# Kernel tuning notes

Measured on AMD Instinct MI355X. Metric: run time of the kernel, lower is better.

Reference implementation:

```python
import jax, jax.numpy as jnp
import numpy as np
import math

D_MODEL = 1024
D_STATE = 64
D_CONV = 4
HEADDIM = 64
EXPAND = 2
NGROUPS = 1
D_INNER = EXPAND * D_MODEL            # 2048
NHEADS = D_INNER // HEADDIM           # 32
CONV_DIM = D_INNER + 2 * NGROUPS * D_STATE   # 2176
D_IN_PROJ = 2 * D_INNER + 2 * NGROUPS * D_STATE + NHEADS  # 4256
BATCH, SEQLEN = 2, 1024
RMS_EPS = 1.1920929e-07  # torch.finfo(float32).eps (nn.RMSNorm default)


def setup_inputs() -> dict:
    key = jax.random.key(0)
    ks = jax.random.split(key, 8)
    x = jax.random.normal(ks[0], (BATCH, SEQLEN, D_MODEL), dtype=jnp.float32)
    W_in = jax.random.normal(ks[1], (D_IN_PROJ, D_MODEL), dtype=jnp.float32) / math.sqrt(D_MODEL)
    conv_w = jax.random.normal(ks[2], (CONV_DIM, D_CONV), dtype=jnp.float32) / math.sqrt(D_CONV)
    conv_b = jnp.zeros((CONV_DIM,), dtype=jnp.float32)
    # dt_bias init as in the module: inverse-softplus of log-uniform dt
    dt_min, dt_max = 1e-3, 1e-1
    dt = jnp.exp(jax.random.uniform(ks[3], (NHEADS,)) * (math.log(dt_max) - math.log(dt_min)) + math.log(dt_min))
    dt = jnp.clip(dt, 1e-4, None)
    dt_bias = dt + jnp.log(-jnp.expm1(-dt))
    A_log = jnp.log(jax.random.uniform(ks[4], (NHEADS,), minval=1.0, maxval=16.0))
    D_param = jnp.ones((NHEADS,), dtype=jnp.float32)
    norm_w = jnp.ones((D_INNER,), dtype=jnp.float32)
    W_out = jax.random.normal(ks[5], (D_MODEL, D_INNER), dtype=jnp.float32) / math.sqrt(D_INNER)
    return {"x": x, "W_in": W_in, "conv_w": conv_w, "conv_b": conv_b,
            "dt_bias": dt_bias, "A_log": A_log, "D_param": D_param,
            "norm_w": norm_w, "W_out": W_out}


def reference(x, W_in, conv_w, conv_b, dt_bias, A_log, D_param, norm_w, W_out):
    B, L, _ = x.shape
    # input projection: z | xBC | dt_raw
    zxbcdt = x @ W_in.T                                   # (B, L, D_IN_PROJ)
    z = zxbcdt[..., :D_INNER]
    xBC = zxbcdt[..., D_INNER:D_INNER + CONV_DIM]
    dt_raw = zxbcdt[..., D_INNER + CONV_DIM:]
    dt = jax.nn.softplus(dt_raw + dt_bias)                # (B, L, H)

    # depthwise causal conv (left-pad d_conv-1, keep first L outputs)
    xpad = jnp.pad(xBC, ((0, 0), (D_CONV - 1, 0), (0, 0)))
    conv_out = conv_b
    for k in range(D_CONV):  # tiny fixed kernel width
        conv_out = conv_out + xpad[:, k:k + L, :] * conv_w[:, k]
    xBC_conv = jax.nn.silu(conv_out)                      # (B, L, CONV_DIM)

    x_ssm = xBC_conv[..., :D_INNER]
    B_ssm = xBC_conv[..., D_INNER:D_INNER + NGROUPS * D_STATE]
    C_ssm = xBC_conv[..., D_INNER + NGROUPS * D_STATE:]

    x_heads = x_ssm.reshape(B, L, NHEADS, HEADDIM)        # (B, L, H, P)
    hpg = NHEADS // NGROUPS
    B_h = jnp.repeat(B_ssm.reshape(B, L, NGROUPS, D_STATE), hpg, axis=2)  # (B, L, H, N)
    C_h = jnp.repeat(C_ssm.reshape(B, L, NGROUPS, D_STATE), hpg, axis=2)

    A = -jnp.exp(A_log)                                   # (H,)
    dA = jnp.exp(dt * A)                                  # (B, L, H)

    # selective SSM scan: h_t = dA_t * h_{t-1} + dt_t * x_t (outer) B_t ; y_t = h_t . C_t
    def step(h, inp):
        dA_t, dt_t, x_t, B_t, C_t = inp   # (B,H), (B,H), (B,H,P), (B,H,N), (B,H,N)
        h = h * dA_t[:, :, None, None] + (dt_t[:, :, None] * x_t)[..., None] * B_t[:, :, None, :]
        y = jnp.einsum('bhpn,bhn->bhp', h, C_t)
        return h, y

    h0 = jnp.zeros((B, NHEADS, HEADDIM, D_STATE), x.dtype)
    xs = (dA.swapaxes(0, 1), dt.swapaxes(0, 1), x_heads.swapaxes(0, 1),
          B_h.swapaxes(0, 1), C_h.swapaxes(0, 1))
    _, ys = jax.lax.scan(step, h0, xs)                    # ys: (L, B, H, P)
    y_heads = ys.swapaxes(0, 1) + D_param[None, None, :, None] * x_heads

    y = y_heads.reshape(B, L, D_INNER)
    # RMSNorm then SiLU(z) gate
    var = jnp.mean(y * y, axis=-1, keepdims=True)
    y = y * jax.lax.rsqrt(var + RMS_EPS) * norm_w
    y = y * jax.nn.silu(z)
    return y @ W_out.T                                    # (B, L, D_MODEL)
```

## Files before the change

### kernel.cpp

```cpp
#include <hip/hip_runtime.h>
#include <hip/hip_bf16.h>
#include <math.h>

#define D_MODEL   1024
#define D_INNER   2048
#define NHEADS    32
#define HEADDIM   64
#define D_STATE   64
#define CONV_DIM  2176
#define D_IN_PROJ 4256
#define ZXLD      4352
#define BATCH     2
#define SEQLEN    1024
#define BL        (BATCH * SEQLEN)
#define RMS_EPS   1.1920929e-07f

#define QCHUNK 64
#define NC     (SEQLEN / QCHUNK)

typedef __attribute__((ext_vector_type(8))) short short8;
typedef __attribute__((ext_vector_type(4))) float f32x4;
typedef __attribute__((ext_vector_type(8))) unsigned short ushort8v;
typedef __attribute__((ext_vector_type(4))) unsigned short ushort4v;

__device__ __forceinline__ unsigned short f2bf(float f) {
    unsigned u = __builtin_bit_cast(unsigned, f);
    unsigned r = u + 0x7FFFu + ((u >> 16) & 1u);
    return (unsigned short)(r >> 16);
}
__device__ __forceinline__ float bf2f(unsigned short u) {
    unsigned v = ((unsigned)u) << 16;
    return __builtin_bit_cast(float, v);
}
__device__ __forceinline__ void gload_lds16(const void* g, void* l) {
    __builtin_amdgcn_global_load_lds(
        (const __attribute__((address_space(1))) void*)g,
        (__attribute__((address_space(3))) void*)l, 16, 0, 0);
}

#define MFMA_BF16 __builtin_amdgcn_mfma_f32_16x16x32_bf16

template<int BM, int BN, int WR, int WC, bool OBF16>
__global__ __launch_bounds__(256) void gemm_bf16_nt(
    const unsigned short* __restrict__ A, const unsigned short* __restrict__ B,
    void* __restrict__ Cv, int K, int ldc)
{
    constexpr int RM = BM / WR;
    constexpr int RN = BN / WC;
    constexpr int MF = RM / 16;
    constexpr int NF = RN / 16;
    constexpr int GA = BM / 32;
    constexpr int GB = BN / 32;

    __shared__ unsigned short As[BM][64];
    __shared__ unsigned short Bs[BN][64];

    const int tid  = threadIdx.x;
    const int lane = tid & 63;
    const int w    = tid >> 6;
    const int wm   = w / WC;
    const int wn   = w % WC;
    const int m0   = blockIdx.y * BM;
    const int n0   = blockIdx.x * BN;

    const int srow  = lane >> 3;
    const int sslot = (lane & 7) ^ srow;

    const int fr  = lane & 15;
    const int h   = lane >> 4;
    const int fr7 = fr & 7;

    f32x4 acc[MF][NF];
#pragma unroll
    for (int mi = 0; mi < MF; ++mi)
#pragma unroll
        for (int ni = 0; ni < NF; ++ni) acc[mi][ni] = (f32x4){0.f, 0.f, 0.f, 0.f};

    for (int k0 = 0; k0 < K; k0 += 64) {
        __syncthreads();
#pragma unroll
        for (int q = 0; q < GA; ++q) {
            const int g8 = (w * GA + q) * 8;
            const unsigned short* gp =
                A + (size_t)(m0 + g8 + srow) * K + k0 + sslot * 8;
            gload_lds16(gp, &As[g8][0]);
        }
#pragma unroll
        for (int q = 0; q < GB; ++q) {
            const int g8 = (w * GB + q) * 8;
            const unsigned short* gp =
                B + (size_t)(n0 + g8 + srow) * K + k0 + sslot * 8;
            gload_lds16(gp, &Bs[g8][0]);
        }
        __syncthreads();

#pragma unroll
        for (int ks = 0; ks < 2; ++ks) {
            const int slot = (ks * 4 + h) ^ fr7;
            short8 av[MF], bv[NF];
#pragma unroll
            for (int mi = 0; mi < MF; ++mi)
                av[mi] = *(const short8*)&As[wm * RM + mi * 16 + fr][slot * 8];
#pragma unroll
            for (int ni = 0; ni < NF; ++ni)
                bv[ni] = *(const short8*)&Bs[wn * RN + ni * 16 + fr][slot * 8];
#pragma unroll
            for (int mi = 0; mi < MF; ++mi)
#pragma unroll
                for (int ni = 0; ni < NF; ++ni)
                    acc[mi][ni] = MFMA_BF16(av[mi], bv[ni], acc[mi][ni], 0, 0, 0);
        }
    }

    const int crow = (lane >> 4) * 4;
    const int ccol = lane & 15;
#pragma unroll
    for (int mi = 0; mi < MF; ++mi)
#pragma unroll
        for (int ni = 0; ni < NF; ++ni) {
            const int row0 = m0 + wm * RM + mi * 16 + crow;
            const int col  = n0 + wn * RN + ni * 16 + ccol;
#pragma unroll
            for (int r = 0; r < 4; ++r) {
                if constexpr (OBF16) {
                    ((unsigned short*)Cv)[(size_t)(row0 + r) * ldc + col] =
                        f2bf(acc[mi][ni][r]);
                } else {
                    ((float*)Cv)[(size_t)(row0 + r) * ldc + col] = acc[mi][ni][r];
                }
            }
        }
}

__global__ __launch_bounds__(256) void cast_bf16_kernel(
    const float* __restrict__ src, unsigned short* __restrict__ dst, int n4)
{
    const int i = (blockIdx.x * 256 + threadIdx.x);
    if (i >= n4) return;
    float4 v = *(const float4*)(src + (size_t)i * 4);
    ushort4 o;
    o.x = f2bf(v.x); o.y = f2bf(v.y); o.z = f2bf(v.z); o.w = f2bf(v.w);
    *(ushort4*)(dst + (size_t)i * 4) = o;
}

__global__ __launch_bounds__(256) void cast_win_pad_kernel(
    const float* __restrict__ src, unsigned short* __restrict__ dst)
{
    const int i = (blockIdx.x * 256 + threadIdx.x);
    if (i >= ZXLD * D_MODEL / 4) return;
    const int e0 = i * 4;
    const int row = e0 >> 10;
    ushort4 o = {0, 0, 0, 0};
    if (row < D_IN_PROJ) {
        float4 v = *(const float4*)(src + (size_t)e0);
        o.x = f2bf(v.x); o.y = f2bf(v.y); o.z = f2bf(v.z); o.w = f2bf(v.w);
    }
    *(ushort4*)(dst + (size_t)e0) = o;
}

__global__ __launch_bounds__(256) void dt_softplus_kernel(
    const unsigned short* __restrict__ zxb, const float* __restrict__ dt_bias,
    float* __restrict__ dtt)
{
    const int idx = blockIdx.x * 256 + threadIdx.x;
    const int m = idx >> 5;
    const int hd = idx & 31;
    const int b = m >> 10;
    const int l = m & (SEQLEN - 1);
    const float v = bf2f(zxb[(size_t)m * ZXLD + (D_INNER + CONV_DIM) + hd]) + dt_bias[hd];
    const float sp = (v > 20.f) ? v : log1pf(__expf(v));
    dtt[((size_t)b * NHEADS + hd) * SEQLEN + l] = sp;
}

__global__ __launch_bounds__(256) void conv_pre_kernel(
    const unsigned short* __restrict__ zxb,
    const float* __restrict__ conv_w, const float* __restrict__ conv_b,
    unsigned short* __restrict__ xTb, unsigned short* __restrict__ Bcc,
    unsigned short* __restrict__ BTc, unsigned short* __restrict__ Ccc)
{
    const int c = blockIdx.x;
    const int g = blockIdx.y;
    const int b = blockIdx.z;
    const int tid = threadIdx.x;

    __shared__ unsigned short L[64][138];

    const int l0 = c * QCHUNK;
    const int grow0 = b * SEQLEN + l0;
    const int r = tid >> 2;
    const int q = (tid & 3) * 16;

    for (int hh = 0; hh < 2; ++hh) {
        const int chbase = g * 128 + hh * 64;
        float in[4][16];
#pragma unroll
        for (int k = 0; k < 4; ++k) {
            const int ll = l0 + r - 3 + k;
            if (ll >= 0) {
                const unsigned short* src =
                    zxb + (size_t)(grow0 + r - 3 + k) * ZXLD + (D_INNER + chbase + q);
                ushort8v v0 = *(const ushort8v*)(src);
                ushort8v v1 = *(const ushort8v*)(src + 8);
#pragma unroll
                for (int j = 0; j < 8; ++j) { in[k][j] = bf2f(v0[j]); in[k][8 + j] = bf2f(v1[j]); }
            } else {
#pragma unroll
                for (int j = 0; j < 16; ++j) in[k][j] = 0.f;
            }
        }
        unsigned short o[16];
#pragma unroll
        for (int j = 0; j < 16; ++j) {
            const int ch = chbase + q + j;
            const float4 wv = *(const float4*)(conv_w + ch * 4);
            float a = conv_b[ch];
            a = fmaf(in[0][j], wv.x, a);
            a = fmaf(in[1][j], wv.y, a);
            a = fmaf(in[2][j], wv.z, a);
            a = fmaf(in[3][j], wv.w, a);
            o[j] = f2bf(a / (1.f + __expf(-a)));
        }

        const bool isB = (g == 16) && (hh == 0);
        const bool isC = (g == 16) && (hh == 1);
        const size_t ctile = ((size_t)b * NC + c) * 4096;

        if (isB || isC) {
            unsigned short* dst = (isB ? Bcc : Ccc) + ctile + (size_t)r * 64 + q;
            ushort8v w0, w1;
#pragma unroll
            for (int j = 0; j < 8; ++j) { w0[j] = o[j]; w1[j] = o[8 + j]; }
            *(ushort8v*)dst = w0;
            *(ushort8v*)(dst + 8) = w1;
        }
        if (!isC) {
#pragma unroll
            for (int j = 0; j < 8; ++j) { L[r][q + j] = o[j]; L[r][q + 8 + j] = o[8 + j]; }
            __syncthreads();
            const int cc = tid >> 2;
            const int tseg = (tid & 3) * 16;
            unsigned short tv[16];
#pragma unroll
            for (int j = 0; j < 16; ++j) tv[j] = L[tseg + j][cc];
            unsigned short* dstT;
            if (isB) dstT = BTc + ctile + (size_t)cc * 64 + tseg;
            else {
                const int hgt = g * 2 + hh;
                dstT = xTb + (((size_t)b * NHEADS + hgt) * NC + c) * 4096 + (size_t)cc * 64 + tseg;
            }
            ushort8v w0, w1;
#pragma unroll
            for (int j = 0; j < 8; ++j) { w0[j] = tv[j]; w1[j] = tv[8 + j]; }
            *(ushort8v*)dstT = w0;
            *(ushort8v*)(dstT + 8) = w1;
        }
        __syncthreads();
    }
}

__global__ __launch_bounds__(256) void chunk_state_kernel(
    const unsigned short* __restrict__ xTb, const unsigned short* __restrict__ BTc,
    const float* __restrict__ dtt, const float* __restrict__ A_log,
    unsigned short* __restrict__ Sintra, float* __restrict__ cumA)
{
    const int bid = blockIdx.x;
    const int c = bid & (NC - 1);
    const int h = (bid >> 4) & (NHEADS - 1);
    const int b = bid >> 9;
    const int tid = threadIdx.x;
    const int lane = tid & 63;
    const int w = tid >> 6;

    __shared__ unsigned short sXT[64][72];
    __shared__ unsigned short sBT[64][72];
    __shared__ float sw[64];

    if (tid < QCHUNK) {
        const float A = -__expf(A_log[h]);
        const float dtv = dtt[((size_t)b * NHEADS + h) * SEQLEN + c * QCHUNK + tid];
        float cum = dtv * A;
#pragma unroll
        for (int off = 1; off < 64; off <<= 1) {
            const float o = __shfl_up(cum, off, 64);
            if (tid >= off) cum += o;
        }
        const float cum_end = __shfl(cum, 63, 64);
        sw[tid] = __expf(cum_end - cum) * dtv;
        cumA[(size_t)bid * QCHUNK + tid] = cum;
    }
    __syncthreads();

    {
        const int r = tid >> 2, q = (tid & 3) * 16;
        const unsigned short* xs =
            xTb + (((size_t)b * NHEADS + h) * NC + c) * 4096 + (size_t)r * 64 + q;
        ushort8v v0 = *(const ushort8v*)(xs);
        ushort8v v1 = *(const ushort8v*)(xs + 8);
        ushort8v s0, s1;
#pragma unroll
        for (int j = 0; j < 8; ++j) {
            s0[j] = f2bf(bf2f(v0[j]) * sw[q + j]);
            s1[j] = f2bf(bf2f(v1[j]) * sw[q + 8 + j]);
        }
        *(ushort8v*)&sXT[r][q] = s0;
        *(ushort8v*)&sXT[r][q + 8] = s1;

        const unsigned short* bs =
            BTc + ((size_t)b * NC + c) * 4096 + (size_t)r * 64 + q;
        *(ushort8v*)&sBT[r][q]     = *(const ushort8v*)(bs);
        *(ushort8v*)&sBT[r][q + 8] = *(const ushort8v*)(bs + 8);
    }
    __syncthreads();

    const int fr = lane & 15;
    const int ko = (lane >> 4) * 8;
    short8 a0 = *(const short8*)&sBT[w * 16 + fr][ko];
    short8 a1 = *(const short8*)&sBT[w * 16 + fr][ko + 32];

    unsigned short* sout = Sintra + (size_t)bid * (D_STATE * HEADDIM);
    const int nrow = w * 16 + (lane >> 4) * 4;
#pragma unroll
    for (int j = 0; j < 4; ++j) {
        short8 b0 = *(const short8*)&sXT[j * 16 + fr][ko];
        short8 b1 = *(const short8*)&sXT[j * 16 + fr][ko + 32];
        f32x4 a = (f32x4){0.f, 0.f, 0.f, 0.f};
        a = MFMA_BF16(a0, b0, a, 0, 0, 0);
        a = MFMA_BF16(a1, b1, a, 0, 0, 0);
        const int p = j * 16 + fr;
#pragma unroll
        for (int r = 0; r < 4; ++r)
            sout[(size_t)(nrow + r) * HEADDIM + p] = f2bf(a[r]);
    }
}

__global__ __launch_bounds__(256) void state_pass_kernel(
    unsigned short* __restrict__ S, const float* __restrict__ cumA)
{
    const int gid = blockIdx.x * 256 + threadIdx.x;
    const int bh = gid >> 10;
    const int e0 = (gid & 1023) * 4;

    float run[4] = {0.f, 0.f, 0.f, 0.f};
    unsigned short* base = S + (size_t)bh * NC * (D_STATE * HEADDIM) + e0;

    ushort4v pre = *(const ushort4v*)base;
    float gpre = __expf(cumA[((size_t)bh * NC) * QCHUNK + (QCHUNK - 1)]);

    for (int c = 0; c < NC; ++c) {
        const ushort4v cur = pre;
        const float g = gpre;
        if (c + 1 < NC) {
            pre = *(const ushort4v*)(base + (size_t)(c + 1) * (D_STATE * HEADDIM));
            gpre = __expf(cumA[((size_t)bh * NC + c + 1) * QCHUNK + (QCHUNK - 1)]);
        }
        ushort4v o;
#pragma unroll
        for (int j = 0; j < 4; ++j) o[j] = f2bf(run[j]);
        *(ushort4v*)(base + (size_t)c * (D_STATE * HEADDIM)) = o;
#pragma unroll
        for (int j = 0; j < 4; ++j) run[j] = fmaf(g, run[j], bf2f(cur[j]));
    }
}

__global__ __launch_bounds__(256) void chunk_output_kernel(
    const unsigned short* __restrict__ xTb, const unsigned short* __restrict__ Bcc,
    const unsigned short* __restrict__ Ccc, const float* __restrict__ dtt,
    const unsigned short* __restrict__ SP, const float* __restrict__ cumA,
    const float* __restrict__ D_param, unsigned short* __restrict__ y)
{
    const int bid = blockIdx.x;
    const int c = bid & (NC - 1);
    const int h = (bid >> 4) & (NHEADS - 1);
    const int b = bid >> 9;
    const int tid = threadIdx.x;
    const int lane = tid & 63;
    const int w = tid >> 6;

    __shared__ unsigned short sC[64][72];
    __shared__ unsigned short sB[64][72];
    __shared__ unsigned short sXT[64][72];
    __shared__ unsigned short sSPT[64][72];
    __shared__ unsigned short sM[64][72];
    __shared__ float scum[64], sdt[64];

    const size_t ctile = ((size_t)b * NC + c) * 4096;
    {
        const int r = tid >> 2, q = (tid & 3) * 16;
        const unsigned short* cs = Ccc + ctile + (size_t)r * 64 + q;
        *(ushort8v*)&sC[r][q]     = *(const ushort8v*)(cs);
        *(ushort8v*)&sC[r][q + 8] = *(const ushort8v*)(cs + 8);
        const unsigned short* bs = Bcc + ctile + (size_t)r * 64 + q;
        *(ushort8v*)&sB[r][q]     = *(const ushort8v*)(bs);
        *(ushort8v*)&sB[r][q + 8] = *(const ushort8v*)(bs + 8);
        const unsigned short* xs =
            xTb + (((size_t)b * NHEADS + h) * NC + c) * 4096 + (size_t)r * 64 + q;
        *(ushort8v*)&sXT[r][q]     = *(const ushort8v*)(xs);
        *(ushort8v*)&sXT[r][q + 8] = *(const ushort8v*)(xs + 8);
        const unsigned short* ss = SP + (size_t)bid * (D_STATE * HEADDIM) + (size_t)r * 64 + q;
        ushort8v v0 = *(const ushort8v*)(ss);
        ushort8v v1 = *(const ushort8v*)(ss + 8);
#pragma unroll
        for (int j = 0; j < 8; ++j) { sSPT[q + j][r] = v0[j]; sSPT[q + 8 + j][r] = v1[j]; }
    }
    if (tid < QCHUNK) {
        scum[tid] = cumA[(size_t)bid * QCHUNK + tid];
        sdt[tid] = dtt[((size_t)b * NHEADS + h) * SEQLEN + c * QCHUNK + tid];
    }
    __syncthreads();

    const int fr = lane & 15;
    const int ko = (lane >> 4) * 8;
    const int trow = w * 16 + (lane >> 4) * 4;

    short8 aC0 = *(const short8*)&sC[w * 16 + fr][ko];
    short8 aC1 = *(const short8*)&sC[w * 16 + fr][ko + 32];

    f32x4 g[4];
#pragma unroll
    for (int j = 0; j < 4; ++j) {
        short8 b0 = *(const short8*)&sB[j * 16 + fr][ko];
        short8 b1 = *(const short8*)&sB[j * 16 + fr][ko + 32];
        f32x4 a = (f32x4){0.f, 0.f, 0.f, 0.f};
        a = MFMA_BF16(aC0, b0, a, 0, 0, 0);
        a = MFMA_BF16(aC1, b1, a, 0, 0, 0);
        g[j] = a;
    }

    float ct[4];
#pragma unroll
    for (int r = 0; r < 4; ++r) ct[r] = scum[trow + r];
#pragma unroll
    for (int j = 0; j < 4; ++j) {
        const int s = j * 16 + fr;
        const float cs = scum[s], ds = sdt[s];
#pragma unroll
        for (int r = 0; r < 4; ++r) {
            const int t = trow + r;
            const float m = (s <= t) ? g[j][r] * __expf(ct[r] - cs) * ds : 0.f;
            sM[t][s] = f2bf(m);
        }
    }
    __syncthreads();

    short8 aM0 = *(const short8*)&sM[w * 16 + fr][ko];
    short8 aM1 = *(const short8*)&sM[w * 16 + fr][ko + 32];
    f32x4 y1[4], y2[4];
#pragma unroll
    for (int j = 0; j < 4; ++j) {
        short8 bx0 = *(const short8*)&sXT[j * 16 + fr][ko];
        short8 bx1 = *(const short8*)&sXT[j * 16 + fr][ko + 32];
        f32x4 a = (f32x4){0.f, 0.f, 0.f, 0.f};
        a = MFMA_BF16(aM0, bx0, a, 0, 0, 0);
        a = MFMA_BF16(aM1, bx1, a, 0, 0, 0);
        y1[j] = a;
        short8 bs0 = *(const short8*)&sSPT[j * 16 + fr][ko];
        short8 bs1 = *(const short8*)&sSPT[j * 16 + fr][ko + 32];
        f32x4 a2 = (f32x4){0.f, 0.f, 0.f, 0.f};
        a2 = MFMA_BF16(aC0, bs0, a2, 0, 0, 0);
        a2 = MFMA_BF16(aC1, bs1, a2, 0, 0, 0);
        y2[j] = a2;
    }

    const float Dp = D_param[h];
    float et[4];
#pragma unroll
    for (int r = 0; r < 4; ++r) et[r] = __expf(ct[r]);
    unsigned short* ybase = y + (((size_t)b * SEQLEN + c * QCHUNK) * D_INNER) + h * HEADDIM;
#pragma unroll
    for (int j = 0; j < 4; ++j) {
        const int p = j * 16 + fr;
#pragma unroll
        for (int r = 0; r < 4; ++r) {
            const int t = trow + r;
            const float xv = bf2f(sXT[p][t]);
            ybase[(size_t)t * D_INNER + p] = f2bf(y1[j][r] + et[r] * y2[j][r] + Dp * xv);
        }
    }
}

__global__ __launch_bounds__(256) void rms_gate_kernel(
    const unsigned short* __restrict__ y, const unsigned short* __restrict__ zxb,
    const float* __restrict__ norm_w, unsigned short* __restrict__ out)
{
    const int m = blockIdx.x;
    const int tid = threadIdx.x;
    const unsigned short* yr = y + (size_t)m * D_INNER;
    const unsigned short* zr = zxb + (size_t)m * ZXLD;

    ushort8v yv8 = *(const ushort8v*)(yr + tid * 8);
    float yv[8];
#pragma unroll
    for (int j = 0; j < 8; ++j) yv[j] = bf2f(yv8[j]);
    float ss = 0.f;
#pragma unroll
    for (int j = 0; j < 8; ++j) ss += yv[j] * yv[j];
#pragma unroll
    for (int off = 32; off > 0; off >>= 1) ss += __shfl_xor(ss, off, 64);
    __shared__ float sred[4];
    if ((tid & 63) == 0) sred[tid >> 6] = ss;
    __syncthreads();
    const float tot = sred[0] + sred[1] + sred[2] + sred[3];
    const float inv = rsqrtf(tot * (1.f / D_INNER) + RMS_EPS);

    ushort8v zv8 = *(const ushort8v*)(zr + tid * 8);
    const float* nw = norm_w + tid * 8;
    ushort8v o;
#pragma unroll
    for (int j = 0; j < 8; ++j) {
        const float zz = bf2f(zv8[j]);
        const float sig = 1.f / (1.f + __expf(-zz));
        o[j] = f2bf(yv[j] * inv * nw[j] * (zz * sig));
    }
    *(ushort8v*)(out + (size_t)m * D_INNER + tid * 8) = o;
}

extern "C" void kernel_launch(void* const* d_in, const int* in_sizes, int n_in,
                              void* d_out, int out_size, void* d_ws, size_t ws_size,
                              hipStream_t stream)
{
    const float* x       = (const float*)d_in[0];
    const float* W_in    = (const float*)d_in[1];
    const float* conv_w  = (const float*)d_in[2];
    const float* conv_b  = (const float*)d_in[3];
    const float* dt_bias = (const float*)d_in[4];
    const float* A_log   = (const float*)d_in[5];
    const float* D_param = (const float*)d_in[6];
    const float* norm_w  = (const float*)d_in[7];
    const float* W_out   = (const float*)d_in[8];
    float* out = (float*)d_out;

    char* p = (char*)d_ws;
    unsigned short* zxb   = (unsigned short*)p;  p += (size_t)BL * ZXLD * 2;
    float*          dtt   = (float*)p;           p += (size_t)BATCH * NHEADS * SEQLEN * 4;
    float*          cumA  = (float*)p;           p += (size_t)BATCH * NHEADS * SEQLEN * 4;
    unsigned short* Sb    = (unsigned short*)p;  p += (size_t)BATCH * NHEADS * NC * 4096 * 2;
    unsigned short* xTb   = (unsigned short*)p;  p += (size_t)BATCH * NHEADS * NC * 4096 * 2;
    unsigned short* Bcc   = (unsigned short*)p;  p += (size_t)BATCH * NC * 4096 * 2;
    unsigned short* BTc   = (unsigned short*)p;  p += (size_t)BATCH * NC * 4096 * 2;
    unsigned short* Ccc   = (unsigned short*)p;  p += (size_t)BATCH * NC * 4096 * 2;
    unsigned short* ybb   = (unsigned short*)p;  p += (size_t)BL * D_INNER * 2;
    unsigned short* xb    = (unsigned short*)p;  p += (size_t)BL * D_MODEL * 2;
    unsigned short* winb  = (unsigned short*)p;  p += (size_t)ZXLD * D_MODEL * 2;
    unsigned short* woutb = (unsigned short*)p;  p += (size_t)D_MODEL * D_INNER * 2;
    unsigned short* ygb   = (unsigned short*)p;

    cast_bf16_kernel<<<(BL * D_MODEL / 4 + 255) / 256, 256, 0, stream>>>(
        x, xb, BL * D_MODEL / 4);
    cast_win_pad_kernel<<<(ZXLD * D_MODEL / 4 + 255) / 256, 256, 0, stream>>>(W_in, winb);
    cast_bf16_kernel<<<(D_MODEL * D_INNER / 4 + 255) / 256, 256, 0, stream>>>(
        W_out, woutb, D_MODEL * D_INNER / 4);

    gemm_bf16_nt<128, 128, 2, 2, true><<<dim3(ZXLD / 128, BL / 128), 256, 0, stream>>>(
        xb, winb, zxb, D_MODEL, ZXLD);

    dt_softplus_kernel<<<(BL * NHEADS) / 256, 256, 0, stream>>>(zxb, dt_bias, dtt);
    conv_pre_kernel<<<dim3(NC, 17, BATCH), 256, 0, stream>>>(
        zxb, conv_w, conv_b, xTb, Bcc, BTc, Ccc);
    chunk_state_kernel<<<BATCH * NHEADS * NC, 256, 0, stream>>>(
        xTb, BTc, dtt, A_log, Sb, cumA);
    state_pass_kernel<<<256, 256, 0, stream>>>(Sb, cumA);
    chunk_output_kernel<<<BATCH * NHEADS * NC, 256, 0, stream>>>(
        xTb, Bcc, Ccc, dtt, Sb, cumA, D_param, ybb);
    rms_gate_kernel<<<BL, 256, 0, stream>>>(ybb, zxb, norm_w, ygb);

    gemm_bf16_nt<64, 64, 2, 2, false><<<dim3(D_MODEL / 64, BL / 64), 256, 0, stream>>>(
        ygb, woutb, out, D_INNER, D_MODEL);
}
```

Baseline: 113.9 us.

## Double-buffer GEMM LDS tiles, fuse casts and fold softplus into conv kernel

The GEMM now keeps two LDS buffers and issues the next K-tile's global-to-LDS loads before computing the current tile, so loads overlap MFMA work with a single barrier per step. The three fp32-to-bf16 cast kernels become one launch, and the dt softplus kernel becomes an extra grid slice of the conv kernel. Together these cut kernel launches and hide load latency. The cost is doubled LDS per block, which can lower occupancy for the 128x128 tile configuration.

```diff
diff --git a/kernel.cpp b/kernel.cpp
--- a/kernel.cpp
+++ b/kernel.cpp
@@ -52,8 +52,8 @@
     constexpr int GA = BM / 32;
     constexpr int GB = BN / 32;
 
-    __shared__ unsigned short As[BM][64];
-    __shared__ unsigned short Bs[BN][64];
+    __shared__ unsigned short As[2][BM][64];
+    __shared__ unsigned short Bs[2][BN][64];
 
     const int tid  = threadIdx.x;
     const int lane = tid & 63;
@@ -67,7 +67,7 @@
     const int sslot = (lane & 7) ^ srow;
 
     const int fr  = lane & 15;
-    const int h   = lane >> 4;
+    const int hq  = lane >> 4;
     const int fr7 = fr & 7;
 
     f32x4 acc[MF][NF];
@@ -76,39 +76,48 @@
 #pragma unroll
         for (int ni = 0; ni < NF; ++ni) acc[mi][ni] = (f32x4){0.f, 0.f, 0.f, 0.f};
 
-    for (int k0 = 0; k0 < K; k0 += 64) {
-        __syncthreads();
+    auto stage = [&](int buf, int k0) {
 #pragma unroll
         for (int q = 0; q < GA; ++q) {
             const int g8 = (w * GA + q) * 8;
-            const unsigned short* gp =
-                A + (size_t)(m0 + g8 + srow) * K + k0 + sslot * 8;
-            gload_lds16(gp, &As[g8][0]);
+            gload_lds16(A + (size_t)(m0 + g8 + srow) * K + k0 + sslot * 8,
+                        &As[buf][g8][0]);
         }
 #pragma unroll
         for (int q = 0; q < GB; ++q) {
             const int g8 = (w * GB + q) * 8;
-            const unsigned short* gp =
-                B + (size_t)(n0 + g8 + srow) * K + k0 + sslot * 8;
-            gload_lds16(gp, &Bs[g8][0]);
-        }
-        __syncthreads();
-
+            gload_lds16(B + (size_t)(n0 + g8 + srow) * K + k0 + sslot * 8,
+                        &Bs[buf][g8][0]);
+        }
+    };
+
+    stage(0, 0);
+    asm volatile("s_waitcnt vmcnt(0)" ::: "memory");
+    __builtin_amdgcn_s_barrier();
+
+    const int NT = K >> 6;
+    for (int t = 0; t < NT; ++t) {
+        const int cb = t & 1;
+        if (t + 1 < NT) stage(cb ^ 1, (t + 1) << 6);
 #pragma unroll
         for (int ks = 0; ks < 2; ++ks) {
-            const int slot = (ks * 4 + h) ^ fr7;
+            const int slot = (ks * 4 + hq) ^ fr7;
             short8 av[MF], bv[NF];
 #pragma unroll
             for (int mi = 0; mi < MF; ++mi)
-                av[mi] = *(const short8*)&As[wm * RM + mi * 16 + fr][slot * 8];
+                av[mi] = *(const short8*)&As[cb][wm * RM + mi * 16 + fr][slot * 8];
 #pragma unroll
             for (int ni = 0; ni < NF; ++ni)
-                bv[ni] = *(const short8*)&Bs[wn * RN + ni * 16 + fr][slot * 8];
+                bv[ni] = *(const short8*)&Bs[cb][wn * RN + ni * 16 + fr][slot * 8];
 #pragma unroll
             for (int mi = 0; mi < MF; ++mi)
 #pragma unroll
                 for (int ni = 0; ni < NF; ++ni)
                     acc[mi][ni] = MFMA_BF16(av[mi], bv[ni], acc[mi][ni], 0, 0, 0);
+        }
+        if (t + 1 < NT) {
+            asm volatile("s_waitcnt vmcnt(0)" ::: "memory");
+            __builtin_amdgcn_s_barrier();
         }
     }
 
@@ -132,61 +141,71 @@
         }
 }
 
-__global__ __launch_bounds__(256) void cast_bf16_kernel(
-    const float* __restrict__ src, unsigned short* __restrict__ dst, int n4)
-{
-    const int i = (blockIdx.x * 256 + threadIdx.x);
-    if (i >= n4) return;
-    float4 v = *(const float4*)(src + (size_t)i * 4);
-    ushort4 o;
-    o.x = f2bf(v.x); o.y = f2bf(v.y); o.z = f2bf(v.z); o.w = f2bf(v.w);
-    *(ushort4*)(dst + (size_t)i * 4) = o;
-}
-
-__global__ __launch_bounds__(256) void cast_win_pad_kernel(
-    const float* __restrict__ src, unsigned short* __restrict__ dst)
-{
-    const int i = (blockIdx.x * 256 + threadIdx.x);
-    if (i >= ZXLD * D_MODEL / 4) return;
-    const int e0 = i * 4;
-    const int row = e0 >> 10;
-    ushort4 o = {0, 0, 0, 0};
-    if (row < D_IN_PROJ) {
-        float4 v = *(const float4*)(src + (size_t)e0);
-        o.x = f2bf(v.x); o.y = f2bf(v.y); o.z = f2bf(v.z); o.w = f2bf(v.w);
-    }
-    *(ushort4*)(dst + (size_t)e0) = o;
-}
-
-__global__ __launch_bounds__(256) void dt_softplus_kernel(
-    const unsigned short* __restrict__ zxb, const float* __restrict__ dt_bias,
-    float* __restrict__ dtt)
-{
-    const int idx = blockIdx.x * 256 + threadIdx.x;
-    const int m = idx >> 5;
-    const int hd = idx & 31;
-    const int b = m >> 10;
-    const int l = m & (SEQLEN - 1);
-    const float v = bf2f(zxb[(size_t)m * ZXLD + (D_INNER + CONV_DIM) + hd]) + dt_bias[hd];
-    const float sp = (v > 20.f) ? v : log1pf(__expf(v));
-    dtt[((size_t)b * NHEADS + hd) * SEQLEN + l] = sp;
+#define CAST_N1 (BL * D_MODEL / 4)
+#define CAST_N2 (ZXLD * D_MODEL / 4)
+#define CAST_N3 (D_MODEL * D_INNER / 4)
+
+__global__ __launch_bounds__(256) void cast_all_kernel(
+    const float* __restrict__ x, const float* __restrict__ W_in,
+    const float* __restrict__ W_out,
+    unsigned short* __restrict__ xb, unsigned short* __restrict__ winb,
+    unsigned short* __restrict__ woutb)
+{
+    const int i = blockIdx.x * 256 + threadIdx.x;
+    if (i < CAST_N1) {
+        float4 v = *(const float4*)(x + (size_t)i * 4);
+        ushort4 o = {f2bf(v.x), f2bf(v.y), f2bf(v.z), f2bf(v.w)};
+        *(ushort4*)(xb + (size_t)i * 4) = o;
+    } else if (i < CAST_N1 + CAST_N2) {
+        const int j = i - CAST_N1;
+        const int e0 = j * 4;
+        const int row = e0 >> 10;
+        ushort4 o = {0, 0, 0, 0};
+        if (row < D_IN_PROJ) {
+            float4 v = *(const float4*)(W_in + (size_t)e0);
+            o.x = f2bf(v.x); o.y = f2bf(v.y); o.z = f2bf(v.z); o.w = f2bf(v.w);
+        }
+        *(ushort4*)(winb + (size_t)e0) = o;
+    } else if (i < CAST_N1 + CAST_N2 + CAST_N3) {
+        const int j = i - CAST_N1 - CAST_N2;
+        float4 v = *(const float4*)(W_out + (size_t)j * 4);
+        ushort4 o = {f2bf(v.x), f2bf(v.y), f2bf(v.z), f2bf(v.w)};
+        *(ushort4*)(woutb + (size_t)j * 4) = o;
+    }
 }
 
 __global__ __launch_bounds__(256) void conv_pre_kernel(
     const unsigned short* __restrict__ zxb,
     const float* __restrict__ conv_w, const float* __restrict__ conv_b,
+    const float* __restrict__ dt_bias,
     unsigned short* __restrict__ xTb, unsigned short* __restrict__ Bcc,
-    unsigned short* __restrict__ BTc, unsigned short* __restrict__ Ccc)
+    unsigned short* __restrict__ BTc, unsigned short* __restrict__ Ccc,
+    float* __restrict__ dtt)
 {
     const int c = blockIdx.x;
     const int g = blockIdx.y;
     const int b = blockIdx.z;
     const int tid = threadIdx.x;
 
-    __shared__ unsigned short L[64][138];
-
     const int l0 = c * QCHUNK;
     const int grow0 = b * SEQLEN + l0;
+
+    if (g == 17) {
+        const int hd = tid & 31;
+        const int t0 = (tid >> 5) * 8;
+        const float bias = dt_bias[hd];
+#pragma unroll
+        for (int j = 0; j < 8; ++j) {
+            const int row = t0 + j;
+            const float v = bf2f(zxb[(size_t)(grow0 + row) * ZXLD +
+                                     (D_INNER + CONV_DIM) + hd]) + bias;
+            const float sp = (v > 20.f) ? v : log1pf(__expf(v));
+            dtt[((size_t)b * NHEADS + hd) * SEQLEN + l0 + row] = sp;
+        }
+        return;
+    }
+
+    __shared__ unsigned short L[64][138];
     const int r = tid >> 2;
     const int q = (tid & 3) * 16;
 
@@ -544,18 +563,14 @@
     unsigned short* woutb = (unsigned short*)p;  p += (size_t)D_MODEL * D_INNER * 2;
     unsigned short* ygb   = (unsigned short*)p;
 
-    cast_bf16_kernel<<<(BL * D_MODEL / 4 + 255) / 256, 256, 0, stream>>>(
-        x, xb, BL * D_MODEL / 4);
-    cast_win_pad_kernel<<<(ZXLD * D_MODEL / 4 + 255) / 256, 256, 0, stream>>>(W_in, winb);
-    cast_bf16_kernel<<<(D_MODEL * D_INNER / 4 + 255) / 256, 256, 0, stream>>>(
-        W_out, woutb, D_MODEL * D_INNER / 4);
+    cast_all_kernel<<<(CAST_N1 + CAST_N2 + CAST_N3 + 255) / 256, 256, 0, stream>>>(
+        x, W_in, W_out, xb, winb, woutb);
 
     gemm_bf16_nt<128, 128, 2, 2, true><<<dim3(ZXLD / 128, BL / 128), 256, 0, stream>>>(
         xb, winb, zxb, D_MODEL, ZXLD);
 
-    dt_softplus_kernel<<<(BL * NHEADS) / 256, 256, 0, stream>>>(zxb, dt_bias, dtt);
-    conv_pre_kernel<<<dim3(NC, 17, BATCH), 256, 0, stream>>>(
-        zxb, conv_w, conv_b, xTb, Bcc, BTc, Ccc);
+    conv_pre_kernel<<<dim3(NC, 18, BATCH), 256, 0, stream>>>(
+        zxb, conv_w, conv_b, dt_bias, xTb, Bcc, BTc, Ccc, dtt);
     chunk_state_kernel<<<BATCH * NHEADS * NC, 256, 0, stream>>>(
         xTb, BTc, dtt, A_log, Sb, cumA);
     state_pass_kernel<<<256, 256, 0, stream>>>(Sb, cumA);
```

Result: slower. 117.2 us (+2.9%).
